# Kernel optimization log

Measured on AMD Instinct MI355X. Metric: run time of the kernel, lower is better.

The kernel has to match this reference:

```python
import jax, jax.numpy as jnp
import numpy as np

DIM = 256
NUM_HEADS = 8
HEAD_DIM = DIM // NUM_HEADS
SCALE = 1.0 / DIM ** 0.5  # NOTE: source scales by 1/sqrt(dim), not 1/sqrt(head_dim)


def setup_inputs() -> dict:
    key = jax.random.key(0)
    k_x, k_wqkv, k_wout = jax.random.split(key, 3)
    x = jax.random.normal(k_x, (4, 2048, DIM), dtype=jnp.float32)
    # xavier_uniform for Linear(dim, 3*dim): limit = sqrt(6/(fan_in+fan_out))
    lim_qkv = float(np.sqrt(6.0 / (DIM + 3 * DIM)))
    w_qkv = jax.random.uniform(k_wqkv, (3 * DIM, DIM), minval=-lim_qkv, maxval=lim_qkv, dtype=jnp.float32)
    b_qkv = jnp.zeros((3 * DIM,), dtype=jnp.float32)
    lim_out = float(np.sqrt(6.0 / (DIM + DIM)))
    w_out = jax.random.uniform(k_wout, (DIM, DIM), minval=-lim_out, maxval=lim_out, dtype=jnp.float32)
    b_out = jnp.zeros((DIM,), dtype=jnp.float32)
    return {"x": x, "w_qkv": w_qkv, "b_qkv": b_qkv, "w_out": w_out, "b_out": b_out}


def reference(x, w_qkv, b_qkv, w_out, b_out):
    B, N, C = x.shape
    H, D = NUM_HEADS, C // NUM_HEADS
    qkv = x @ w_qkv.T + b_qkv                       # [B, N, 3C]
    qkv = qkv.reshape(B, N, 3, H, D)
    q = qkv[:, :, 0].transpose(0, 2, 1, 3)          # [B, H, N, D]
    k = qkv[:, :, 1].transpose(0, 2, 1, 3)
    v = qkv[:, :, 2].transpose(0, 2, 1, 3)
    attn = jnp.einsum("bhnd,bhmd->bhnm", q, k) * SCALE  # [B, H, N, N]
    attn = jax.nn.softmax(attn, axis=-1)
    z = jnp.einsum("bhnm,bhmd->bhnd", attn, v)      # [B, H, N, D]
    z = z.transpose(0, 2, 1, 3).reshape(B, N, C)
    return z @ w_out.T + b_out
```

## Files before the change

### kernel.cpp

```cpp
#include <hip/hip_runtime.h>


#define SEQ 2048
#define BATCH 4
#define NHEADS 8
#define HDIM 32
#define DIMC 256
#define SCALE_LOG2E 0.09016844005556021f

typedef __attribute__((ext_vector_type(8))) short short8;
typedef __attribute__((ext_vector_type(4))) float f32x4;

union BF8 { unsigned u[4]; short8 s8; };

__device__ __forceinline__ unsigned pk2bf(float a, float b) {
    union { float f; unsigned u; } ua, ub;
    ua.f = a; ub.f = b;
    return __builtin_amdgcn_perm(ub.u + 0x8000u, ua.u + 0x8000u, 0x07060302u);
}
__device__ __forceinline__ short f2bf(float a) {
    union { float f; unsigned u; } x; x.f = a;
    return (short)((x.u + 0x8000u) >> 16);
}

__global__ __launch_bounds__(256) void qkv_mfma(const float* __restrict__ X,
                                                const float* __restrict__ W,
                                                const float* __restrict__ bias,
                                                short* __restrict__ Q,
                                                short* __restrict__ Kd,
                                                short* __restrict__ V) {
    __shared__ __align__(16) short Xs[64][40];
    __shared__ __align__(16) short Ws[64][40];
    __shared__ __align__(16) short Cs[64][72];
    const int m0 = blockIdx.y * 64, n0 = blockIdx.x * 64;
    const int tid = threadIdx.x;
    const int w = tid >> 6, lane = tid & 63;
    const int m = lane & 15, g = lane >> 4;
    const int srow = tid >> 2, scol = (tid & 3) * 8;

    f32x4 acc[4] = {};

    for (int kt = 0; kt < DIMC; kt += 32) {
        const float* xp = &X[(size_t)(m0 + srow) * DIMC + kt + scol];
        const float* wp = &W[(size_t)(n0 + srow) * DIMC + kt + scol];
        float4 x0 = *(const float4*)xp, x1 = *(const float4*)(xp + 4);
        float4 w0 = *(const float4*)wp, w1 = *(const float4*)(wp + 4);
        __syncthreads();
        BF8 cx, cw;
        cx.u[0] = pk2bf(x0.x, x0.y); cx.u[1] = pk2bf(x0.z, x0.w);
        cx.u[2] = pk2bf(x1.x, x1.y); cx.u[3] = pk2bf(x1.z, x1.w);
        cw.u[0] = pk2bf(w0.x, w0.y); cw.u[1] = pk2bf(w0.z, w0.w);
        cw.u[2] = pk2bf(w1.x, w1.y); cw.u[3] = pk2bf(w1.z, w1.w);
        *(short8*)&Xs[srow][scol] = cx.s8;
        *(short8*)&Ws[srow][scol] = cw.s8;
        __syncthreads();
        short8 afrag = *(const short8*)&Xs[w * 16 + m][g * 8];
#pragma unroll
        for (int t = 0; t < 4; t++) {
            short8 bfrag = *(const short8*)&Ws[t * 16 + m][g * 8];
            acc[t] = __builtin_amdgcn_mfma_f32_16x16x32_bf16(afrag, bfrag, acc[t], 0, 0, 0);
        }
    }

    float bv[4];
#pragma unroll
    for (int t = 0; t < 4; t++) bv[t] = bias[n0 + t * 16 + m];

    const int which = n0 >> 8;
    const int bidx = m0 >> 11, ntok0 = m0 & 2047;
    const int h0 = (n0 & 255) >> 5;

    __syncthreads();
    if (which != 2) {
        const float qs = (which == 0) ? SCALE_LOG2E : 1.0f;
#pragma unroll
        for (int t = 0; t < 4; t++)
#pragma unroll
            for (int r = 0; r < 4; r++)
                Cs[w * 16 + g * 4 + r][t * 16 + m] = f2bf((acc[t][r] + bv[t]) * qs);
        __syncthreads();
        short* dst = (which == 0) ? Q : Kd;
#pragma unroll
        for (int hh = 0; hh < 2; hh++) {
            int tok = tid >> 2, d = (tid & 3) * 8;
            short8 val = *(const short8*)&Cs[tok][hh * 32 + d];
            size_t off = ((size_t)((bidx * NHEADS + h0 + hh) * SEQ) + ntok0 + tok) * HDIM + d;
            *(short8*)&dst[off] = val;
        }
    } else {
#pragma unroll
        for (int t = 0; t < 4; t++)
#pragma unroll
            for (int r = 0; r < 4; r++)
                Cs[t * 16 + m][w * 16 + g * 4 + r] = f2bf(acc[t][r] + bv[t]);
        __syncthreads();
#pragma unroll
        for (int half = 0; half < 2; half++) {
            int c = (tid >> 3) + half * 32, tok = (tid & 7) * 8;
            short8 val = *(const short8*)&Cs[c][tok];
            int hh = c >> 5, d = c & 31;
            size_t off = ((size_t)((bidx * NHEADS + h0 + hh) * HDIM) + d) * SEQ + ntok0 + tok;
            *(short8*)&V[off] = val;
        }
    }
}

__global__ __launch_bounds__(256) void attn_mfma(const short* __restrict__ Q,
                                                 const short* __restrict__ K,
                                                 const short* __restrict__ V,
                                                 short* __restrict__ Zb) {
    __shared__ __align__(16) short Ks[64][40];
    __shared__ __align__(16) short Vs[32][72];
    __shared__ __align__(16) float Ps[4][16][68];

    const int bh = blockIdx.y;
    const int b = bh >> 3, h = bh & 7;
    const int q0 = blockIdx.x * 64;
    const short* qb = Q + (size_t)bh * SEQ * HDIM;
    const short* kb = K + (size_t)bh * SEQ * HDIM;
    const short* vbase = V + (size_t)bh * HDIM * SEQ;
    const int tid = threadIdx.x;
    const int w = tid >> 6, lane = tid & 63;
    const int m = lane & 15, g = lane >> 4;

    const short8 qfrag = *(const short8*)(qb + (size_t)(q0 + w * 16 + m) * HDIM + g * 8);
    const short8 ones = {0x3F80, 0x3F80, 0x3F80, 0x3F80, 0x3F80, 0x3F80, 0x3F80, 0x3F80};

    f32x4 o0 = {0.f, 0.f, 0.f, 0.f};
    f32x4 o1 = {0.f, 0.f, 0.f, 0.f};
    f32x4 ol = {0.f, 0.f, 0.f, 0.f};

    const int kr = tid >> 2, kc = (tid & 3) * 8;
    const int vr = tid >> 3, vc = (tid & 7) * 8;

    for (int k0 = 0; k0 < SEQ; k0 += 64) {
        short8 kload = *(const short8*)(kb + (size_t)(k0 + kr) * HDIM + kc);
        short8 vload = *(const short8*)(vbase + (size_t)vr * SEQ + k0 + vc);
        __syncthreads();
        *(short8*)&Ks[kr][kc] = kload;
        *(short8*)&Vs[vr][vc] = vload;
        __syncthreads();

        f32x4 s[4];
#pragma unroll
        for (int t = 0; t < 4; t++) {
            short8 bfrag = *(const short8*)&Ks[t * 16 + m][g * 8];
            f32x4 zero = {0.f, 0.f, 0.f, 0.f};
            s[t] = __builtin_amdgcn_mfma_f32_16x16x32_bf16(qfrag, bfrag, zero, 0, 0, 0);
        }

#pragma unroll
        for (int t = 0; t < 4; t++)
#pragma unroll
            for (int r = 0; r < 4; r++)
                Ps[w][g * 4 + r][t * 16 + m] = __builtin_amdgcn_exp2f(s[t][r]);

#pragma unroll
        for (int c = 0; c < 2; c++) {
            f32x4 pa = *(const f32x4*)&Ps[w][m][c * 32 + g * 8];
            f32x4 pb = *(const f32x4*)&Ps[w][m][c * 32 + g * 8 + 4];
            BF8 cv;
            cv.u[0] = pk2bf(pa[0], pa[1]); cv.u[1] = pk2bf(pa[2], pa[3]);
            cv.u[2] = pk2bf(pb[0], pb[1]); cv.u[3] = pk2bf(pb[2], pb[3]);
            short8 vb0 = *(const short8*)&Vs[m][c * 32 + g * 8];
            short8 vb1 = *(const short8*)&Vs[m + 16][c * 32 + g * 8];
            o0 = __builtin_amdgcn_mfma_f32_16x16x32_bf16(cv.s8, vb0, o0, 0, 0, 0);
            o1 = __builtin_amdgcn_mfma_f32_16x16x32_bf16(cv.s8, vb1, o1, 0, 0, 0);
            ol = __builtin_amdgcn_mfma_f32_16x16x32_bf16(cv.s8, ones, ol, 0, 0, 0);
        }
    }

    const int row = q0 + w * 16 + g * 4;
#pragma unroll
    for (int r = 0; r < 4; r++) {
        float inv = __builtin_amdgcn_rcpf(ol[r]);
        size_t zo = ((size_t)(b * SEQ + row + r)) * DIMC + h * HDIM + m;
        Zb[zo] = f2bf(o0[r] * inv);
        Zb[zo + 16] = f2bf(o1[r] * inv);
    }
}

__global__ __launch_bounds__(256) void out_mfma(const short* __restrict__ Zb,
                                                const float* __restrict__ W,
                                                const float* __restrict__ bias,
                                                float* __restrict__ C) {
    __shared__ __align__(16) short As_[64][40];
    __shared__ __align__(16) short Ws[64][40];
    const int m0 = blockIdx.y * 64, n0 = blockIdx.x * 64;
    const int tid = threadIdx.x;
    const int w = tid >> 6, lane = tid & 63;
    const int m = lane & 15, g = lane >> 4;
    const int srow = tid >> 2, scol = (tid & 3) * 8;

    f32x4 acc[4] = {};

    for (int kt = 0; kt < DIMC; kt += 32) {
        short8 a8 = *(const short8*)&Zb[(size_t)(m0 + srow) * DIMC + kt + scol];
        const float* wp = &W[(size_t)(n0 + srow) * DIMC + kt + scol];
        float4 w0 = *(const float4*)wp, w1 = *(const float4*)(wp + 4);
        __syncthreads();
        BF8 cw;
        cw.u[0] = pk2bf(w0.x, w0.y); cw.u[1] = pk2bf(w0.z, w0.w);
        cw.u[2] = pk2bf(w1.x, w1.y); cw.u[3] = pk2bf(w1.z, w1.w);
        *(short8*)&As_[srow][scol] = a8;
        *(short8*)&Ws[srow][scol] = cw.s8;
        __syncthreads();
        short8 afrag = *(const short8*)&As_[w * 16 + m][g * 8];
#pragma unroll
        for (int t = 0; t < 4; t++) {
            short8 bfrag = *(const short8*)&Ws[t * 16 + m][g * 8];
            acc[t] = __builtin_amdgcn_mfma_f32_16x16x32_bf16(afrag, bfrag, acc[t], 0, 0, 0);
        }
    }

    float bv[4];
#pragma unroll
    for (int t = 0; t < 4; t++) bv[t] = bias[n0 + t * 16 + m];
#pragma unroll
    for (int t = 0; t < 4; t++)
#pragma unroll
        for (int r = 0; r < 4; r++)
            C[(size_t)(m0 + w * 16 + g * 4 + r) * DIMC + n0 + t * 16 + m] = acc[t][r] + bv[t];
}

extern "C" void kernel_launch(void* const* d_in, const int* in_sizes, int n_in,
                              void* d_out, int out_size, void* d_ws, size_t ws_size,
                              hipStream_t stream) {
    const float* x     = (const float*)d_in[0];
    const float* w_qkv = (const float*)d_in[1];
    const float* b_qkv = (const float*)d_in[2];
    const float* w_out = (const float*)d_in[3];
    const float* b_out = (const float*)d_in[4];
    float* out = (float*)d_out;

    const size_t HSZ = (size_t)BATCH * NHEADS * SEQ * HDIM;
    short* qw = (short*)d_ws;
    short* kw = qw + HSZ;
    short* vw = kw + HSZ;
    short* zb = vw + HSZ;

    qkv_mfma<<<dim3(12, 128), 256, 0, stream>>>(x, w_qkv, b_qkv, qw, kw, vw);
    attn_mfma<<<dim3(32, 32), 256, 0, stream>>>(qw, kw, vw, zb);
    out_mfma<<<dim3(4, 128), 256, 0, stream>>>(zb, w_out, b_out, out);
}
```

Baseline: 131.8 us.

## Pre-convert to bf16, enlarge GEMM tiles, and stream attention without shared memory

A new kernel converts x and both weight matrices to bf16 up front. The QKV and output GEMMs now use 128-row tiles with a 64-wide K step and more MFMAs per wave, which cuts global reloads and barriers. The attention kernel drops LDS staging: each wave loads K and V fragments straight from global memory, handles 32 query rows, and swaps the QK operand order so the exp'd scores land directly in the register layout needed for the PV MFMA. That removes the P round-trip through shared memory. The cost is an extra launch plus workspace traffic for the conversion, and redundant global K/V loads across waves that now rely on cache.

```diff
diff --git a/kernel.cpp b/kernel.cpp
--- a/kernel.cpp
+++ b/kernel.cpp
@@ -23,204 +23,274 @@
     return (short)((x.u + 0x8000u) >> 16);
 }
 
-__global__ __launch_bounds__(256) void qkv_mfma(const float* __restrict__ X,
-                                                const float* __restrict__ W,
+#define NX (BATCH * SEQ * DIMC)
+#define NQW (3 * DIMC * DIMC)
+#define NOW (DIMC * DIMC)
+
+__global__ __launch_bounds__(256) void cvt_bf16(const float* __restrict__ x,
+                                                const float* __restrict__ wq,
+                                                const float* __restrict__ wo,
+                                                short* __restrict__ xb,
+                                                short* __restrict__ wqb,
+                                                short* __restrict__ wob) {
+    int i = (blockIdx.x * 256 + threadIdx.x) * 4;
+    const float* src;
+    short* dst;
+    int off;
+    if (i < NX) { src = x; dst = xb; off = i; }
+    else if (i < NX + NQW) { src = wq; dst = wqb; off = i - NX; }
+    else { src = wo; dst = wob; off = i - NX - NQW; }
+    float4 v = *(const float4*)&src[off];
+    uint2 p;
+    p.x = pk2bf(v.x, v.y);
+    p.y = pk2bf(v.z, v.w);
+    *(uint2*)&dst[off] = p;
+}
+
+__global__ __launch_bounds__(256) void qkv_mfma(const short* __restrict__ Xb,
+                                                const short* __restrict__ Wb,
                                                 const float* __restrict__ bias,
                                                 short* __restrict__ Q,
                                                 short* __restrict__ Kd,
                                                 short* __restrict__ V) {
-    __shared__ __align__(16) short Xs[64][40];
-    __shared__ __align__(16) short Ws[64][40];
-    __shared__ __align__(16) short Cs[64][72];
-    const int m0 = blockIdx.y * 64, n0 = blockIdx.x * 64;
+    __shared__ __align__(16) union SM {
+        struct { short A[128][72]; short B[128][72]; } ab;
+        short C[128][136];
+    } sm;
+    const int m0 = blockIdx.y * 128, bx = blockIdx.x;
     const int tid = threadIdx.x;
     const int w = tid >> 6, lane = tid & 63;
     const int m = lane & 15, g = lane >> 4;
-    const int srow = tid >> 2, scol = (tid & 3) * 8;
-
-    f32x4 acc[4] = {};
-
-    for (int kt = 0; kt < DIMC; kt += 32) {
-        const float* xp = &X[(size_t)(m0 + srow) * DIMC + kt + scol];
-        const float* wp = &W[(size_t)(n0 + srow) * DIMC + kt + scol];
-        float4 x0 = *(const float4*)xp, x1 = *(const float4*)(xp + 4);
-        float4 w0 = *(const float4*)wp, w1 = *(const float4*)(wp + 4);
-        __syncthreads();
-        BF8 cx, cw;
-        cx.u[0] = pk2bf(x0.x, x0.y); cx.u[1] = pk2bf(x0.z, x0.w);
-        cx.u[2] = pk2bf(x1.x, x1.y); cx.u[3] = pk2bf(x1.z, x1.w);
-        cw.u[0] = pk2bf(w0.x, w0.y); cw.u[1] = pk2bf(w0.z, w0.w);
-        cw.u[2] = pk2bf(w1.x, w1.y); cw.u[3] = pk2bf(w1.z, w1.w);
-        *(short8*)&Xs[srow][scol] = cx.s8;
-        *(short8*)&Ws[srow][scol] = cw.s8;
-        __syncthreads();
-        short8 afrag = *(const short8*)&Xs[w * 16 + m][g * 8];
-#pragma unroll
-        for (int t = 0; t < 4; t++) {
-            short8 bfrag = *(const short8*)&Ws[t * 16 + m][g * 8];
-            acc[t] = __builtin_amdgcn_mfma_f32_16x16x32_bf16(afrag, bfrag, acc[t], 0, 0, 0);
-        }
-    }
-
+    const int wr = w >> 1, wc = w & 1;
+    const int srow = tid >> 1, scol = (tid & 1) * 32;
+
+    f32x4 acc[4][4] = {};
+
+    for (int kt = 0; kt < DIMC; kt += 64) {
+        short8 a8[4], b8[4];
+#pragma unroll
+        for (int i = 0; i < 4; i++) {
+            a8[i] = *(const short8*)&Xb[(size_t)(m0 + srow) * DIMC + kt + scol + i * 8];
+            b8[i] = *(const short8*)&Wb[(size_t)(bx * 128 + srow) * DIMC + kt + scol + i * 8];
+        }
+        __syncthreads();
+#pragma unroll
+        for (int i = 0; i < 4; i++) {
+            *(short8*)&sm.ab.A[srow][scol + i * 8] = a8[i];
+            *(short8*)&sm.ab.B[srow][scol + i * 8] = b8[i];
+        }
+        __syncthreads();
+#pragma unroll
+        for (int kk = 0; kk < 2; kk++) {
+            short8 af[4], bf[4];
+#pragma unroll
+            for (int mt = 0; mt < 4; mt++) af[mt] = *(const short8*)&sm.ab.A[wr * 64 + mt * 16 + m][kk * 32 + g * 8];
+#pragma unroll
+            for (int nt = 0; nt < 4; nt++) bf[nt] = *(const short8*)&sm.ab.B[wc * 64 + nt * 16 + m][kk * 32 + g * 8];
+#pragma unroll
+            for (int mt = 0; mt < 4; mt++)
+#pragma unroll
+                for (int nt = 0; nt < 4; nt++)
+                    acc[mt][nt] = __builtin_amdgcn_mfma_f32_16x16x32_bf16(af[mt], bf[nt], acc[mt][nt], 0, 0, 0);
+        }
+    }
+
+    const int which = bx >> 1;
+    const int h0 = (bx & 1) * 4;
+    const int bidx = blockIdx.y >> 4;
+    const int ntok0 = (blockIdx.y & 15) * 128;
     float bv[4];
 #pragma unroll
-    for (int t = 0; t < 4; t++) bv[t] = bias[n0 + t * 16 + m];
-
-    const int which = n0 >> 8;
-    const int bidx = m0 >> 11, ntok0 = m0 & 2047;
-    const int h0 = (n0 & 255) >> 5;
+    for (int nt = 0; nt < 4; nt++) bv[nt] = bias[bx * 128 + wc * 64 + nt * 16 + m];
 
     __syncthreads();
     if (which != 2) {
         const float qs = (which == 0) ? SCALE_LOG2E : 1.0f;
 #pragma unroll
-        for (int t = 0; t < 4; t++)
-#pragma unroll
-            for (int r = 0; r < 4; r++)
-                Cs[w * 16 + g * 4 + r][t * 16 + m] = f2bf((acc[t][r] + bv[t]) * qs);
+        for (int mt = 0; mt < 4; mt++)
+#pragma unroll
+            for (int nt = 0; nt < 4; nt++)
+#pragma unroll
+                for (int r = 0; r < 4; r++)
+                    sm.C[wr * 64 + mt * 16 + g * 4 + r][wc * 64 + nt * 16 + m] =
+                        f2bf((acc[mt][nt][r] + bv[nt]) * qs);
         __syncthreads();
         short* dst = (which == 0) ? Q : Kd;
-#pragma unroll
-        for (int hh = 0; hh < 2; hh++) {
-            int tok = tid >> 2, d = (tid & 3) * 8;
-            short8 val = *(const short8*)&Cs[tok][hh * 32 + d];
-            size_t off = ((size_t)((bidx * NHEADS + h0 + hh) * SEQ) + ntok0 + tok) * HDIM + d;
-            *(short8*)&dst[off] = val;
+        const int tok = tid >> 1, d0 = (tid & 1) * 16;
+#pragma unroll
+        for (int hh = 0; hh < 4; hh++) {
+            size_t o = ((size_t)((bidx * NHEADS + h0 + hh) * SEQ) + ntok0 + tok) * HDIM + d0;
+            *(short8*)&dst[o] = *(const short8*)&sm.C[tok][hh * 32 + d0];
+            *(short8*)&dst[o + 8] = *(const short8*)&sm.C[tok][hh * 32 + d0 + 8];
         }
     } else {
 #pragma unroll
-        for (int t = 0; t < 4; t++)
-#pragma unroll
-            for (int r = 0; r < 4; r++)
-                Cs[t * 16 + m][w * 16 + g * 4 + r] = f2bf(acc[t][r] + bv[t]);
-        __syncthreads();
-#pragma unroll
-        for (int half = 0; half < 2; half++) {
-            int c = (tid >> 3) + half * 32, tok = (tid & 7) * 8;
-            short8 val = *(const short8*)&Cs[c][tok];
-            int hh = c >> 5, d = c & 31;
-            size_t off = ((size_t)((bidx * NHEADS + h0 + hh) * HDIM) + d) * SEQ + ntok0 + tok;
-            *(short8*)&V[off] = val;
-        }
-    }
-}
-
-__global__ __launch_bounds__(256) void attn_mfma(const short* __restrict__ Q,
-                                                 const short* __restrict__ K,
-                                                 const short* __restrict__ V,
-                                                 short* __restrict__ Zb) {
-    __shared__ __align__(16) short Ks[64][40];
-    __shared__ __align__(16) short Vs[32][72];
-    __shared__ __align__(16) float Ps[4][16][68];
-
+        for (int mt = 0; mt < 4; mt++)
+#pragma unroll
+            for (int nt = 0; nt < 4; nt++) {
+                uint2 p;
+                p.x = pk2bf(acc[mt][nt][0] + bv[nt], acc[mt][nt][1] + bv[nt]);
+                p.y = pk2bf(acc[mt][nt][2] + bv[nt], acc[mt][nt][3] + bv[nt]);
+                *(uint2*)&sm.C[wc * 64 + nt * 16 + m][wr * 64 + mt * 16 + g * 4] = p;
+            }
+        __syncthreads();
+        const int col = tid >> 1, t0 = (tid & 1) * 64;
+        const int hh = col >> 5, d = col & 31;
+        size_t o = ((size_t)((bidx * NHEADS + h0 + hh) * HDIM) + d) * SEQ + ntok0 + t0;
+#pragma unroll
+        for (int c2 = 0; c2 < 8; c2++)
+            *(short8*)&V[o + c2 * 8] = *(const short8*)&sm.C[col][t0 + c2 * 8];
+    }
+}
+
+__global__ __launch_bounds__(256) void attn_stream(const short* __restrict__ Q,
+                                                   const short* __restrict__ K,
+                                                   const short* __restrict__ V,
+                                                   short* __restrict__ Zb) {
     const int bh = blockIdx.y;
     const int b = bh >> 3, h = bh & 7;
-    const int q0 = blockIdx.x * 64;
+    const int q0 = blockIdx.x * 128;
     const short* qb = Q + (size_t)bh * SEQ * HDIM;
     const short* kb = K + (size_t)bh * SEQ * HDIM;
-    const short* vbase = V + (size_t)bh * HDIM * SEQ;
+    const short* vb = V + (size_t)bh * HDIM * SEQ;
     const int tid = threadIdx.x;
     const int w = tid >> 6, lane = tid & 63;
     const int m = lane & 15, g = lane >> 4;
 
-    const short8 qfrag = *(const short8*)(qb + (size_t)(q0 + w * 16 + m) * HDIM + g * 8);
+    short8 qf[2];
+    qf[0] = *(const short8*)(qb + (size_t)(q0 + w * 32 + m) * HDIM + g * 8);
+    qf[1] = *(const short8*)(qb + (size_t)(q0 + w * 32 + 16 + m) * HDIM + g * 8);
+
+    int koff[4];
+#pragma unroll
+    for (int t = 0; t < 4; t++) {
+        int row = 32 * (t >> 1) + ((m >> 2) << 3) + ((t & 1) << 2) + (m & 3);
+        koff[t] = row * HDIM + g * 8;
+    }
+    const int voff0 = m * SEQ + g * 8;
+    const int voff1 = (m + 16) * SEQ + g * 8;
+
+    f32x4 o00 = {0.f, 0.f, 0.f, 0.f}, o01 = {0.f, 0.f, 0.f, 0.f};
+    f32x4 o10 = {0.f, 0.f, 0.f, 0.f}, o11 = {0.f, 0.f, 0.f, 0.f};
+    f32x4 ol0 = {0.f, 0.f, 0.f, 0.f}, ol1 = {0.f, 0.f, 0.f, 0.f};
     const short8 ones = {0x3F80, 0x3F80, 0x3F80, 0x3F80, 0x3F80, 0x3F80, 0x3F80, 0x3F80};
 
-    f32x4 o0 = {0.f, 0.f, 0.f, 0.f};
-    f32x4 o1 = {0.f, 0.f, 0.f, 0.f};
-    f32x4 ol = {0.f, 0.f, 0.f, 0.f};
-
-    const int kr = tid >> 2, kc = (tid & 3) * 8;
-    const int vr = tid >> 3, vc = (tid & 7) * 8;
-
     for (int k0 = 0; k0 < SEQ; k0 += 64) {
-        short8 kload = *(const short8*)(kb + (size_t)(k0 + kr) * HDIM + kc);
-        short8 vload = *(const short8*)(vbase + (size_t)vr * SEQ + k0 + vc);
-        __syncthreads();
-        *(short8*)&Ks[kr][kc] = kload;
-        *(short8*)&Vs[vr][vc] = vload;
-        __syncthreads();
-
-        f32x4 s[4];
-#pragma unroll
-        for (int t = 0; t < 4; t++) {
-            short8 bfrag = *(const short8*)&Ks[t * 16 + m][g * 8];
-            f32x4 zero = {0.f, 0.f, 0.f, 0.f};
-            s[t] = __builtin_amdgcn_mfma_f32_16x16x32_bf16(qfrag, bfrag, zero, 0, 0, 0);
-        }
-
+        short8 kf[4];
 #pragma unroll
         for (int t = 0; t < 4; t++)
-#pragma unroll
-            for (int r = 0; r < 4; r++)
-                Ps[w][g * 4 + r][t * 16 + m] = __builtin_amdgcn_exp2f(s[t][r]);
-
-#pragma unroll
-        for (int c = 0; c < 2; c++) {
-            f32x4 pa = *(const f32x4*)&Ps[w][m][c * 32 + g * 8];
-            f32x4 pb = *(const f32x4*)&Ps[w][m][c * 32 + g * 8 + 4];
-            BF8 cv;
-            cv.u[0] = pk2bf(pa[0], pa[1]); cv.u[1] = pk2bf(pa[2], pa[3]);
-            cv.u[2] = pk2bf(pb[0], pb[1]); cv.u[3] = pk2bf(pb[2], pb[3]);
-            short8 vb0 = *(const short8*)&Vs[m][c * 32 + g * 8];
-            short8 vb1 = *(const short8*)&Vs[m + 16][c * 32 + g * 8];
-            o0 = __builtin_amdgcn_mfma_f32_16x16x32_bf16(cv.s8, vb0, o0, 0, 0, 0);
-            o1 = __builtin_amdgcn_mfma_f32_16x16x32_bf16(cv.s8, vb1, o1, 0, 0, 0);
-            ol = __builtin_amdgcn_mfma_f32_16x16x32_bf16(cv.s8, ones, ol, 0, 0, 0);
-        }
-    }
-
-    const int row = q0 + w * 16 + g * 4;
-#pragma unroll
-    for (int r = 0; r < 4; r++) {
-        float inv = __builtin_amdgcn_rcpf(ol[r]);
-        size_t zo = ((size_t)(b * SEQ + row + r)) * DIMC + h * HDIM + m;
-        Zb[zo] = f2bf(o0[r] * inv);
-        Zb[zo + 16] = f2bf(o1[r] * inv);
-    }
-}
-
-__global__ __launch_bounds__(256) void out_mfma(const short* __restrict__ Zb,
-                                                const float* __restrict__ W,
+            kf[t] = *(const short8*)(kb + (size_t)k0 * HDIM + koff[t]);
+        short8 vf00 = *(const short8*)(vb + voff0 + k0);
+        short8 vf01 = *(const short8*)(vb + voff1 + k0);
+        short8 vf10 = *(const short8*)(vb + voff0 + k0 + 32);
+        short8 vf11 = *(const short8*)(vb + voff1 + k0 + 32);
+
+#pragma unroll
+        for (int qh = 0; qh < 2; qh++) {
+            f32x4 st[4];
+#pragma unroll
+            for (int t = 0; t < 4; t++) {
+                f32x4 z4 = {0.f, 0.f, 0.f, 0.f};
+                st[t] = __builtin_amdgcn_mfma_f32_16x16x32_bf16(kf[t], qh ? qf[1] : qf[0], z4, 0, 0, 0);
+            }
+            BF8 a0, a1;
+#pragma unroll
+            for (int t = 0; t < 2; t++) {
+                a0.u[t * 2 + 0] = pk2bf(__builtin_amdgcn_exp2f(st[t][0]), __builtin_amdgcn_exp2f(st[t][1]));
+                a0.u[t * 2 + 1] = pk2bf(__builtin_amdgcn_exp2f(st[t][2]), __builtin_amdgcn_exp2f(st[t][3]));
+                a1.u[t * 2 + 0] = pk2bf(__builtin_amdgcn_exp2f(st[t + 2][0]), __builtin_amdgcn_exp2f(st[t + 2][1]));
+                a1.u[t * 2 + 1] = pk2bf(__builtin_amdgcn_exp2f(st[t + 2][2]), __builtin_amdgcn_exp2f(st[t + 2][3]));
+            }
+            if (qh == 0) {
+                o00 = __builtin_amdgcn_mfma_f32_16x16x32_bf16(a0.s8, vf00, o00, 0, 0, 0);
+                o01 = __builtin_amdgcn_mfma_f32_16x16x32_bf16(a0.s8, vf01, o01, 0, 0, 0);
+                ol0 = __builtin_amdgcn_mfma_f32_16x16x32_bf16(a0.s8, ones, ol0, 0, 0, 0);
+                o00 = __builtin_amdgcn_mfma_f32_16x16x32_bf16(a1.s8, vf10, o00, 0, 0, 0);
+                o01 = __builtin_amdgcn_mfma_f32_16x16x32_bf16(a1.s8, vf11, o01, 0, 0, 0);
+                ol0 = __builtin_amdgcn_mfma_f32_16x16x32_bf16(a1.s8, ones, ol0, 0, 0, 0);
+            } else {
+                o10 = __builtin_amdgcn_mfma_f32_16x16x32_bf16(a0.s8, vf00, o10, 0, 0, 0);
+                o11 = __builtin_amdgcn_mfma_f32_16x16x32_bf16(a0.s8, vf01, o11, 0, 0, 0);
+                ol1 = __builtin_amdgcn_mfma_f32_16x16x32_bf16(a0.s8, ones, ol1, 0, 0, 0);
+                o10 = __builtin_amdgcn_mfma_f32_16x16x32_bf16(a1.s8, vf10, o10, 0, 0, 0);
+                o11 = __builtin_amdgcn_mfma_f32_16x16x32_bf16(a1.s8, vf11, o11, 0, 0, 0);
+                ol1 = __builtin_amdgcn_mfma_f32_16x16x32_bf16(a1.s8, ones, ol1, 0, 0, 0);
+            }
+        }
+    }
+
+#pragma unroll
+    for (int qh = 0; qh < 2; qh++) {
+        f32x4 oa = qh ? o10 : o00;
+        f32x4 ob = qh ? o11 : o01;
+        f32x4 ll = qh ? ol1 : ol0;
+#pragma unroll
+        for (int r = 0; r < 4; r++) {
+            float inv = __builtin_amdgcn_rcpf(ll[r]);
+            int row = q0 + w * 32 + qh * 16 + g * 4 + r;
+            size_t zo = ((size_t)(b * SEQ + row)) * DIMC + h * HDIM + m;
+            Zb[zo] = f2bf(oa[r] * inv);
+            Zb[zo + 16] = f2bf(ob[r] * inv);
+        }
+    }
+}
+
+__global__ __launch_bounds__(256) void out_mfma(const short* __restrict__ A,
+                                                const short* __restrict__ Wb,
                                                 const float* __restrict__ bias,
                                                 float* __restrict__ C) {
-    __shared__ __align__(16) short As_[64][40];
-    __shared__ __align__(16) short Ws[64][40];
-    const int m0 = blockIdx.y * 64, n0 = blockIdx.x * 64;
+    __shared__ __align__(16) short As[128][72];
+    __shared__ __align__(16) short Bs[64][72];
+    const int m0 = blockIdx.y * 128, n0 = blockIdx.x * 64;
     const int tid = threadIdx.x;
     const int w = tid >> 6, lane = tid & 63;
     const int m = lane & 15, g = lane >> 4;
-    const int srow = tid >> 2, scol = (tid & 3) * 8;
-
-    f32x4 acc[4] = {};
-
-    for (int kt = 0; kt < DIMC; kt += 32) {
-        short8 a8 = *(const short8*)&Zb[(size_t)(m0 + srow) * DIMC + kt + scol];
-        const float* wp = &W[(size_t)(n0 + srow) * DIMC + kt + scol];
-        float4 w0 = *(const float4*)wp, w1 = *(const float4*)(wp + 4);
-        __syncthreads();
-        BF8 cw;
-        cw.u[0] = pk2bf(w0.x, w0.y); cw.u[1] = pk2bf(w0.z, w0.w);
-        cw.u[2] = pk2bf(w1.x, w1.y); cw.u[3] = pk2bf(w1.z, w1.w);
-        *(short8*)&As_[srow][scol] = a8;
-        *(short8*)&Ws[srow][scol] = cw.s8;
-        __syncthreads();
-        short8 afrag = *(const short8*)&As_[w * 16 + m][g * 8];
-#pragma unroll
-        for (int t = 0; t < 4; t++) {
-            short8 bfrag = *(const short8*)&Ws[t * 16 + m][g * 8];
-            acc[t] = __builtin_amdgcn_mfma_f32_16x16x32_bf16(afrag, bfrag, acc[t], 0, 0, 0);
-        }
-    }
-
-    float bv[4];
-#pragma unroll
-    for (int t = 0; t < 4; t++) bv[t] = bias[n0 + t * 16 + m];
-#pragma unroll
-    for (int t = 0; t < 4; t++)
-#pragma unroll
-        for (int r = 0; r < 4; r++)
-            C[(size_t)(m0 + w * 16 + g * 4 + r) * DIMC + n0 + t * 16 + m] = acc[t][r] + bv[t];
+    const int wr = w >> 1, wc = w & 1;
+    const int arow = tid >> 1, acol = (tid & 1) * 32;
+    const int brow = tid >> 2, bcol = (tid & 3) * 16;
+
+    f32x4 acc[4][2] = {};
+
+    for (int kt = 0; kt < DIMC; kt += 64) {
+        short8 a8[4], b8[2];
+#pragma unroll
+        for (int i = 0; i < 4; i++)
+            a8[i] = *(const short8*)&A[(size_t)(m0 + arow) * DIMC + kt + acol + i * 8];
+#pragma unroll
+        for (int i = 0; i < 2; i++)
+            b8[i] = *(const short8*)&Wb[(size_t)(n0 + brow) * DIMC + kt + bcol + i * 8];
+        __syncthreads();
+#pragma unroll
+        for (int i = 0; i < 4; i++) *(short8*)&As[arow][acol + i * 8] = a8[i];
+#pragma unroll
+        for (int i = 0; i < 2; i++) *(short8*)&Bs[brow][bcol + i * 8] = b8[i];
+        __syncthreads();
+#pragma unroll
+        for (int kk = 0; kk < 2; kk++) {
+            short8 af[4], bf2[2];
+#pragma unroll
+            for (int mt = 0; mt < 4; mt++) af[mt] = *(const short8*)&As[wr * 64 + mt * 16 + m][kk * 32 + g * 8];
+#pragma unroll
+            for (int nt = 0; nt < 2; nt++) bf2[nt] = *(const short8*)&Bs[wc * 32 + nt * 16 + m][kk * 32 + g * 8];
+#pragma unroll
+            for (int mt = 0; mt < 4; mt++)
+#pragma unroll
+                for (int nt = 0; nt < 2; nt++)
+                    acc[mt][nt] = __builtin_amdgcn_mfma_f32_16x16x32_bf16(af[mt], bf2[nt], acc[mt][nt], 0, 0, 0);
+        }
+    }
+
+    float bv[2];
+    bv[0] = bias[n0 + wc * 32 + m];
+    bv[1] = bias[n0 + wc * 32 + 16 + m];
+#pragma unroll
+    for (int mt = 0; mt < 4; mt++)
+#pragma unroll
+        for (int nt = 0; nt < 2; nt++)
+#pragma unroll
+            for (int r = 0; r < 4; r++)
+                C[(size_t)(m0 + wr * 64 + mt * 16 + g * 4 + r) * DIMC + n0 + wc * 32 + nt * 16 + m] =
+                    acc[mt][nt][r] + bv[nt];
 }
 
 extern "C" void kernel_launch(void* const* d_in, const int* in_sizes, int n_in,
@@ -234,12 +304,16 @@
     float* out = (float*)d_out;
 
     const size_t HSZ = (size_t)BATCH * NHEADS * SEQ * HDIM;
-    short* qw = (short*)d_ws;
-    short* kw = qw + HSZ;
-    short* vw = kw + HSZ;
-    short* zb = vw + HSZ;
-
-    qkv_mfma<<<dim3(12, 128), 256, 0, stream>>>(x, w_qkv, b_qkv, qw, kw, vw);
-    attn_mfma<<<dim3(32, 32), 256, 0, stream>>>(qw, kw, vw, zb);
-    out_mfma<<<dim3(4, 128), 256, 0, stream>>>(zb, w_out, b_out, out);
-}
+    short* xb  = (short*)d_ws;
+    short* wqb = xb + NX;
+    short* wob = wqb + NQW;
+    short* qw  = wob + NOW;
+    short* kw  = qw + HSZ;
+    short* vw  = kw + HSZ;
+    short* zb  = vw + HSZ;
+
+    cvt_bf16<<<(NX + NQW + NOW) / 1024, 256, 0, stream>>>(x, w_qkv, w_out, xb, wqb, wob);
+    qkv_mfma<<<dim3(6, 64), 256, 0, stream>>>(xb, wqb, b_qkv, qw, kw, vw);
+    attn_stream<<<dim3(16, 32), 256, 0, stream>>>(qw, kw, vw, zb);
+    out_mfma<<<dim3(4, 64), 256, 0, stream>>>(zb, wob, b_out, out);
+}
```

Measured after the change: 132.5 us. Within noise of the previous version (+0.5%).
